# Optimization experiments

Measured on AMD Instinct MI355X. Metric: run time of the kernel, lower is better.

## Reference

```python
import jax, jax.numpy as jnp
import numpy as np

N, E, R = 50000, 400000, 500
X_SIZE = 100
G_SIZE = 100
HID = 64
OUT = 64
HEADS = 2
ALPHA = 0.5
NEG_SLOPE = 0.01  # nn.LeakyReLU default and attention slope
EPS = 1e-12       # F.normalize eps


def _l2norm(x, axis):
    return x / jnp.maximum(jnp.linalg.norm(x, axis=axis, keepdims=True), EPS)


def _xavier(key, shape, gain=1.414):
    fan_in, fan_out = shape[-1], int(np.prod(shape[:-1]))
    std = gain * np.sqrt(2.0 / (fan_in + fan_out))
    return jax.random.normal(key, shape, dtype=jnp.float32) * std


def _att_layer(h, g, row, col, etype, W, b, att, out_size):
    # h: [N, D_h], g: [R, D_g], W: [heads*out, 2*D_h+D_g], att: [1, heads, out]
    n = h.shape[0]
    h_ijk = jnp.concatenate([h[row], h[col], g[etype]], axis=1)      # [E, 2D_h+D_g]
    c_ijk = (h_ijk @ W.T + b).reshape(-1, HEADS, out_size)           # [E, H, O]
    a = jnp.sum(att * c_ijk, axis=2, keepdims=True)                  # [E, H, 1]
    e = jnp.exp(jax.nn.leaky_relu(a, NEG_SLOPE))                     # unnormalized (matches torch exp w/o max-sub)
    denom = jax.ops.segment_sum(e, row, num_segments=n)              # [N, H, 1]
    alpha = e / denom[row]
    # self-edge zeros contribute nothing; segment_sum over num_segments=n is equivalent
    return jax.ops.segment_sum(alpha * c_ijk, col, num_segments=n)   # [N, H, O]


def setup_inputs() -> dict:
    key = jax.random.key(0)
    ks = jax.random.split(key, 20)
    x = jax.random.normal(ks[0], (N, X_SIZE), dtype=jnp.float32)
    g = jax.random.normal(ks[1], (R, G_SIZE), dtype=jnp.float32)
    edge_idx = jax.random.randint(ks[2], (2, E), 0, N)
    edge_type = jax.random.randint(ks[3], (E,), 0, R)
    d1 = 2 * X_SIZE + G_SIZE
    d2 = 2 * HID * HEADS + G_SIZE
    inp = {
        "x": x, "g": g, "edge_idx": edge_idx, "edge_type": edge_type,
        "W1i": _xavier(ks[4], (HEADS * HID, d1)), "b1i": jnp.zeros((HEADS * HID,), jnp.float32),
        "a1i": _xavier(ks[5], (1, HEADS, HID)),
        "W1o": _xavier(ks[6], (HEADS * HID, d1)), "b1o": jnp.zeros((HEADS * HID,), jnp.float32),
        "a1o": _xavier(ks[7], (1, HEADS, HID)),
        "W2i": _xavier(ks[8], (HEADS * OUT, d2)), "b2i": jnp.zeros((HEADS * OUT,), jnp.float32),
        "a2i": _xavier(ks[9], (1, HEADS, OUT)),
        "W2o": _xavier(ks[10], (HEADS * OUT, d2)), "b2o": jnp.zeros((HEADS * OUT,), jnp.float32),
        "a2o": _xavier(ks[11], (1, HEADS, OUT)),
        "We": _xavier(ks[12], (HID, X_SIZE)), "be": jnp.zeros((HID,), jnp.float32),
        "Wr": _xavier(ks[13], (HEADS * HID, G_SIZE)), "br": jnp.zeros((HEADS * HID,), jnp.float32),
    }
    return inp


def reference(x, g, edge_idx, edge_type, W1i, b1i, a1i, W1o, b1o, a1o,
              W2i, b2i, a2i, W2o, b2o, a2o, We, be, Wr, br):
    # x = F.normalize(x, dim=1).detach()
    xn = jax.lax.stop_gradient(_l2norm(x, axis=1))
    row, col = edge_idx[0], edge_idx[1]

    h_in = _att_layer(xn, g, row, col, edge_type, W1i, b1i, a1i, HID)
    h_out = _att_layer(xn, g, col, row, edge_type, W1o, b1o, a1o, HID)
    h = jax.nn.leaky_relu(ALPHA * h_in + (1.0 - ALPHA) * h_out, NEG_SLOPE)
    h = _l2norm(h, axis=2)                                # [N, H, HID]
    h = h.transpose(0, 1, 2).reshape(N, HEADS * HID)      # concat heads

    h_in = _att_layer(h, g, row, col, edge_type, W2i, b2i, a2i, OUT)
    h_out = _att_layer(h, g, col, row, edge_type, W2o, b2o, a2o, OUT)
    h = jax.nn.leaky_relu(ALPHA * h_in + (1.0 - ALPHA) * h_out, NEG_SLOPE)
    h = _l2norm(h, axis=2)                                # [N, H, OUT]

    # EntityLayer: Linear(x)[:, None, :] + h  (requires HID == OUT)
    h_prime = (xn @ We.T + be)[:, None, :] + h            # [N, H, OUT]
    h_prime = h_prime.reshape(N, HEADS * OUT)
    h_prime = _l2norm(h_prime, axis=1)                    # (torch dim=2 bug -> last dim)
    # _merge_heads stores mean but returns input unchanged

    g_prime = g @ Wr.T + br                               # [R, HEADS*HID]
    return h_prime, g_prime
```

## Files before the change

### kernel.cpp

```cpp
#include <hip/hip_runtime.h>

typedef unsigned short u16;
typedef unsigned int u32;
typedef short short8v __attribute__((ext_vector_type(8)));
typedef float float4v __attribute__((ext_vector_type(4)));

#define N_NODES 50000
#define E_EDGES 400000
#define R_REL   500
#define NKEYS   100000
#define SCAN_B  98
#define SEG     ((size_t)N_NODES * 128)

__device__ __forceinline__ float bl(u32 u){ return __uint_as_float(u << 16); }
__device__ __forceinline__ float bh(u32 u){ return __uint_as_float(u & 0xffff0000u); }
__device__ __forceinline__ u16 f2b(float f){
    u32 u = __float_as_uint(f);
    return (u16)((u + 0x7fffu + ((u >> 16) & 1u)) >> 16);
}
__device__ __forceinline__ u32 pk2(float a, float b){ return (u32)f2b(a) | ((u32)f2b(b) << 16); }
__device__ __forceinline__ float lrelu(float x){ return x > 0.f ? x : 0.01f * x; }

__global__ void k_norm_x(const float* __restrict__ x, u16* __restrict__ xnb){
    int wid = threadIdx.x >> 6, l = threadIdx.x & 63;
    int n = blockIdx.x * 4 + wid;
    if (n >= N_NODES) return;
    float v0 = x[(size_t)n * 100 + l];
    float v1 = (l + 64 < 100) ? x[(size_t)n * 100 + 64 + l] : 0.f;
    float ss = v0 * v0 + v1 * v1;
    #pragma unroll
    for (int m = 32; m; m >>= 1) ss += __shfl_xor(ss, m);
    float s = 1.f / fmaxf(sqrtf(ss), 1e-12f);
    xnb[(size_t)n * 128 + l] = f2b(v0 * s);
    xnb[(size_t)n * 128 + 64 + l] = (l + 64 < 100) ? f2b(v1 * s) : (u16)0;
}

__global__ void k_build_wcat(const float* __restrict__ W1i, const float* __restrict__ W1o,
                             const float* __restrict__ W2i, const float* __restrict__ W2o,
                             const float* __restrict__ We,
                             u16* __restrict__ wc1, u16* __restrict__ wc2){
    int idx = blockIdx.x * blockDim.x + threadIdx.x;
    if (idx < 576 * 128){
        int r = idx >> 7, k = idx & 127;
        float v = 0.f;
        if (r < 512){
            int seg = r >> 7, rr = r & 127;
            const float* W = (seg < 2) ? W1i : W1o;
            int off = (seg & 1) ? 100 : 0;
            if (k < 100) v = W[(size_t)rr * 300 + off + k];
        } else {
            int rr = r - 512;
            if (k < 100) v = We[(size_t)rr * 100 + k];
        }
        wc1[idx] = f2b(v);
    } else if (idx < 576 * 128 + 512 * 128){
        int j = idx - 576 * 128;
        int r = j >> 7, k = j & 127;
        int seg = r >> 7, rr = r & 127;
        const float* W = (seg < 2) ? W2i : W2o;
        int off = (seg & 1) ? 128 : 0;
        wc2[j] = f2b(W[(size_t)rr * 356 + off + k]);
    }
}

__global__ void k_pg(const float* __restrict__ g,
                     const float* __restrict__ W1i, const float* __restrict__ W1o,
                     const float* __restrict__ W2i, const float* __restrict__ W2o,
                     const float* __restrict__ b1i, const float* __restrict__ b1o,
                     const float* __restrict__ b2i, const float* __restrict__ b2o,
                     const float* __restrict__ a1i, const float* __restrict__ a1o,
                     const float* __restrict__ a2i, const float* __restrict__ a2o,
                     float* __restrict__ Pg, float* __restrict__ qg){
    int bid = blockIdx.x;
    int r = bid >> 2, t = bid & 3;
    const float *W, *b, *att; int ld, off;
    if (t == 0){ W = W1i; ld = 300; off = 200; b = b1i; att = a1i; }
    else if (t == 1){ W = W1o; ld = 300; off = 200; b = b1o; att = a1o; }
    else if (t == 2){ W = W2i; ld = 356; off = 256; b = b2i; att = a2i; }
    else { W = W2o; ld = 356; off = 256; b = b2o; att = a2o; }
    __shared__ float gs[100];
    __shared__ float red[128];
    int j = threadIdx.x;
    if (j < 100) gs[j] = g[(size_t)r * 100 + j];
    __syncthreads();
    float acc = b[j];
    #pragma unroll 4
    for (int k = 0; k < 100; ++k) acc += gs[k] * W[(size_t)j * ld + off + k];
    Pg[((size_t)t * R_REL + r) * 128 + j] = acc;
    red[j] = att[j] * acc;
    __syncthreads();
    if (j < 2){
        float s = 0.f;
        for (int k = 0; k < 64; ++k) s += red[j * 64 + k];
        qg[((size_t)t * R_REL + r) * 2 + j] = s;
    }
}

__global__ void k_gprime(const float* __restrict__ g, const float* __restrict__ Wr,
                         const float* __restrict__ br, float* __restrict__ out){
    int r = blockIdx.x, j = threadIdx.x;
    __shared__ float gs[100];
    if (j < 100) gs[j] = g[(size_t)r * 100 + j];
    __syncthreads();
    float acc = br[j];
    #pragma unroll 4
    for (int k = 0; k < 100; ++k) acc += gs[k] * Wr[(size_t)j * 100 + k];
    out[(size_t)N_NODES * 128 + (size_t)r * 128 + j] = acc;
}

__launch_bounds__(256)
__global__ void k_gemm(const u16* __restrict__ A, const u16* __restrict__ W,
                       u16* __restrict__ NPt, int M, int NN){
    int l = threadIdx.x & 63, w = threadIdx.x >> 6;
    int rb = blockIdx.x * 64 + w * 16;
    int ar = rb + (l & 15); if (ar >= M) ar = M - 1;
    const u16* Ap = A + (size_t)ar * 128 + (l >> 4) * 8;
    short8v a0 = *(const short8v*)(Ap);
    short8v a1 = *(const short8v*)(Ap + 32);
    short8v a2 = *(const short8v*)(Ap + 64);
    short8v a3 = *(const short8v*)(Ap + 96);
    int ntc = NN >> 4;
    for (int nt = 0; nt < ntc; ++nt){
        const u16* Wp = W + (size_t)(nt * 16 + (l & 15)) * 128 + (l >> 4) * 8;
        short8v b0 = *(const short8v*)(Wp);
        short8v b1 = *(const short8v*)(Wp + 32);
        short8v b2 = *(const short8v*)(Wp + 64);
        short8v b3 = *(const short8v*)(Wp + 96);
        float4v acc = {0.f, 0.f, 0.f, 0.f};
        acc = __builtin_amdgcn_mfma_f32_16x16x32_bf16(a0, b0, acc, 0, 0, 0);
        acc = __builtin_amdgcn_mfma_f32_16x16x32_bf16(a1, b1, acc, 0, 0, 0);
        acc = __builtin_amdgcn_mfma_f32_16x16x32_bf16(a2, b2, acc, 0, 0, 0);
        acc = __builtin_amdgcn_mfma_f32_16x16x32_bf16(a3, b3, acc, 0, 0, 0);
        int cc = nt * 16 + (l & 15);
        int seg = cc >> 7;
        int rr0 = rb + (l >> 4) * 4;
        #pragma unroll
        for (int r = 0; r < 4; ++r){
            int rr = rr0 + r;
            if (rr < M){
                if (seg < 4) NPt[(size_t)seg * SEG + (size_t)rr * 128 + (cc & 127)] = f2b(acc[r]);
                else         NPt[4 * SEG + (size_t)rr * 64 + (cc & 63)] = f2b(acc[r]);
            }
        }
    }
}

__global__ void k_qnode(const u16* __restrict__ NPt,
                        const float* __restrict__ attI, const float* __restrict__ attO,
                        float* __restrict__ q){
    int wid = threadIdx.x >> 6, l = threadIdx.x & 63;
    int n = blockIdx.x * 4 + wid;
    if (n >= N_NODES) return;
    int t = l >> 4, h = (l >> 3) & 1;
    uint4 uv = *(const uint4*)(NPt + (size_t)t * SEG + (size_t)n * 128 + (l & 15) * 8);
    const float* att = ((t < 2) ? attI : attO) + h * 64 + (l & 7) * 8;
    float s = bl(uv.x) * att[0] + bh(uv.x) * att[1] + bl(uv.y) * att[2] + bh(uv.y) * att[3]
            + bl(uv.z) * att[4] + bh(uv.z) * att[5] + bl(uv.w) * att[6] + bh(uv.w) * att[7];
    s += __shfl_xor(s, 1); s += __shfl_xor(s, 2); s += __shfl_xor(s, 4);
    if ((l & 7) == 0) q[(size_t)n * 8 + t * 2 + h] = s;
}

__global__ void k_hist(const int* __restrict__ ei, u32* __restrict__ cnt){
    int e = blockIdx.x * blockDim.x + threadIdx.x;
    if (e >= E_EDGES) return;
    atomicAdd(&cnt[ei[E_EDGES + e]], 1u);
    atomicAdd(&cnt[N_NODES + ei[e]], 1u);
}

__launch_bounds__(1024)
__global__ void k_scan1(const u32* __restrict__ cnt, u32* __restrict__ off, u32* __restrict__ bsum){
    __shared__ u32 sh[1024];
    int t = threadIdx.x, b = blockIdx.x, idx = b * 1024 + t;
    u32 v = cnt[idx];
    sh[t] = v; __syncthreads();
    #pragma unroll
    for (int d = 1; d < 1024; d <<= 1){
        u32 add = (t >= d) ? sh[t - d] : 0;
        __syncthreads();
        sh[t] += add;
        __syncthreads();
    }
    off[idx] = sh[t] - v;
    if (t == 1023) bsum[b] = sh[1023];
}

__global__ void k_scan2(u32* __restrict__ bsum){
    if (threadIdx.x == 0){
        u32 run = 0;
        for (int i = 0; i < SCAN_B; ++i){ u32 t = bsum[i]; bsum[i] = run; run += t; }
    }
}

__launch_bounds__(1024)
__global__ void k_scan3(u32* __restrict__ off, const u32* __restrict__ bsum){
    int idx = blockIdx.x * 1024 + threadIdx.x;
    off[idx] += bsum[blockIdx.x];
}

__global__ void k_pos(const int* __restrict__ ei, const int* __restrict__ ety,
                      u32* __restrict__ cur,
                      u32* __restrict__ Pso, u32* __restrict__ Pss){
    int e = blockIdx.x * blockDim.x + threadIdx.x;
    if (e >= E_EDGES) return;
    u32 row = (u32)ei[e], col = (u32)ei[E_EDGES + e];
    u32 etb = (u32)ety[e] << 20;
    u32 pI = atomicAdd(&cur[col], 1u);
    Pso[pI] = row | etb;  Pss[pI] = col;
    u32 pO = atomicAdd(&cur[N_NODES + row], 1u);
    Pso[pO] = col | etb;  Pss[pO] = row;
}

__global__ void k_edgeA(const u32* __restrict__ Pso, const u32* __restrict__ Pss,
                        const float* __restrict__ q,
                        const float* __restrict__ qgI, const float* __restrict__ qgO,
                        float2* __restrict__ exI, float2* __restrict__ exO){
    int p = blockIdx.x * blockDim.x + threadIdx.x;
    if (p >= 2 * E_EDGES) return;
    u32 so = Pso[p], self = Pss[p];
    u32 oth = so & 0xFFFFF, et = so >> 20;
    u32 row, col;
    if (p < E_EDGES){ row = oth; col = self; } else { row = self; col = oth; }
    const float* qr = q + (size_t)row * 8;
    const float* qc = q + (size_t)col * 8;
    float2 ri, ro;
    ri.x = expf(lrelu(qr[0] + qc[2] + qgI[(size_t)et * 2 + 0]));
    ri.y = expf(lrelu(qr[1] + qc[3] + qgI[(size_t)et * 2 + 1]));
    ro.x = expf(lrelu(qc[4] + qr[6] + qgO[(size_t)et * 2 + 0]));
    ro.y = expf(lrelu(qc[5] + qr[7] + qgO[(size_t)et * 2 + 1]));
    exI[p] = ri;
    exO[p] = ro;
}

__global__ void k_denom(const u32* __restrict__ off,
                        const float2* __restrict__ exI, const float2* __restrict__ exO,
                        float* __restrict__ rdI, float* __restrict__ rdO){
    int n = blockIdx.x * blockDim.x + threadIdx.x;
    if (n >= N_NODES) return;
    float s0 = 0.f, s1 = 0.f;
    for (u32 p = off[N_NODES + n]; p < off[N_NODES + n + 1]; ++p){
        float2 v = exI[p]; s0 += v.x; s1 += v.y;
    }
    rdI[(size_t)n * 2 + 0] = (s0 > 0.f) ? 1.f / s0 : 0.f;
    rdI[(size_t)n * 2 + 1] = (s1 > 0.f) ? 1.f / s1 : 0.f;
    float t0 = 0.f, t1 = 0.f;
    for (u32 p = off[n]; p < off[n + 1]; ++p){
        float2 v = exO[p]; t0 += v.x; t1 += v.y;
    }
    rdO[(size_t)n * 2 + 0] = (t0 > 0.f) ? 1.f / t0 : 0.f;
    rdO[(size_t)n * 2 + 1] = (t1 > 0.f) ? 1.f / t1 : 0.f;
}

__launch_bounds__(256)
__global__ void k_agg(const u32* __restrict__ off,
                      const u32* __restrict__ Pso,
                      const float2* __restrict__ exI, const float2* __restrict__ exO,
                      const u16* __restrict__ NPt,
                      const float* __restrict__ PgI, const float* __restrict__ PgO,
                      const float* __restrict__ rdI, const float* __restrict__ rdO,
                      int final_stage,
                      const u16* __restrict__ NPt1, const float* __restrict__ be,
                      u16* __restrict__ h1b, float* __restrict__ out){
    int wid = threadIdx.x >> 6, l = threadIdx.x & 63;
    int n = blockIdx.x * 4 + wid;
    if (n >= N_NODES) return;
    int h = l >> 5, d0 = l * 2;
    const u16* PaI = NPt;
    const u16* PbI = NPt + SEG;
    const u16* PaO = NPt + 2 * SEG;
    const u16* PbO = NPt + 3 * SEG;
    u32 pbi = *(const u32*)(PbI + (size_t)n * 128 + d0);
    u32 pbo = *(const u32*)(PbO + (size_t)n * 128 + d0);

    float a0 = 0.f, a1 = 0.f, sai = 0.f;
    {
        u32 s0 = off[n], deg = off[n + 1] - s0;
        for (u32 base = 0; base < deg; base += 64){
            u32 k = base + (u32)l;
            u32 so = 0u; float w0 = 0.f, w1 = 0.f;
            if (k < deg){
                u32 idx = s0 + k;
                so = __builtin_nontemporal_load(Pso + idx);
                const float* ep = (const float*)exI + (size_t)idx * 2;
                float e0 = __builtin_nontemporal_load(ep);
                float e1 = __builtin_nontemporal_load(ep + 1);
                u32 oth = so & 0xFFFFFu;
                float2 rd2 = *(const float2*)(rdI + (size_t)oth * 2);
                w0 = e0 * rd2.x; w1 = e1 * rd2.y;
            }
            int cnt = (int)((deg - base < 64u) ? (deg - base) : 64u);
            for (int c = 0; c < cnt; c += 8){
                float wj[8]; u32 pa[8]; float2 gv[8];
                #pragma unroll
                for (int j = 0; j < 8; ++j){
                    u32 s = __shfl(so, c + j);
                    float v0 = __shfl(w0, c + j);
                    float v1 = __shfl(w1, c + j);
                    u32 oth = s & 0xFFFFFu, et = s >> 20;
                    pa[j] = *(const u32*)(PaI + (size_t)oth * 128 + d0);
                    gv[j] = *(const float2*)(PgI + (size_t)et * 128 + d0);
                    wj[j] = h ? v1 : v0;
                }
                #pragma unroll
                for (int j = 0; j < 8; ++j){
                    a0 += wj[j] * (bl(pa[j]) + gv[j].x);
                    a1 += wj[j] * (bh(pa[j]) + gv[j].y);
                    sai += wj[j];
                }
            }
        }
    }
    a0 += sai * bl(pbi);
    a1 += sai * bh(pbi);

    float b0 = 0.f, b1 = 0.f, sao = 0.f;
    {
        u32 s0 = off[N_NODES + n], deg = off[N_NODES + n + 1] - s0;
        for (u32 base = 0; base < deg; base += 64){
            u32 k = base + (u32)l;
            u32 so = 0u; float w0 = 0.f, w1 = 0.f;
            if (k < deg){
                u32 idx = s0 + k;
                so = __builtin_nontemporal_load(Pso + idx);
                const float* ep = (const float*)exO + (size_t)idx * 2;
                float e0 = __builtin_nontemporal_load(ep);
                float e1 = __builtin_nontemporal_load(ep + 1);
                u32 oth = so & 0xFFFFFu;
                float2 rd2 = *(const float2*)(rdO + (size_t)oth * 2);
                w0 = e0 * rd2.x; w1 = e1 * rd2.y;
            }
            int cnt = (int)((deg - base < 64u) ? (deg - base) : 64u);
            for (int c = 0; c < cnt; c += 8){
                float wj[8]; u32 pa[8]; float2 gv[8];
                #pragma unroll
                for (int j = 0; j < 8; ++j){
                    u32 s = __shfl(so, c + j);
                    float v0 = __shfl(w0, c + j);
                    float v1 = __shfl(w1, c + j);
                    u32 oth = s & 0xFFFFFu, et = s >> 20;
                    pa[j] = *(const u32*)(PaO + (size_t)oth * 128 + d0);
                    gv[j] = *(const float2*)(PgO + (size_t)et * 128 + d0);
                    wj[j] = h ? v1 : v0;
                }
                #pragma unroll
                for (int j = 0; j < 8; ++j){
                    b0 += wj[j] * (bl(pa[j]) + gv[j].x);
                    b1 += wj[j] * (bh(pa[j]) + gv[j].y);
                    sao += wj[j];
                }
            }
        }
    }
    b0 += sao * bl(pbo);
    b1 += sao * bh(pbo);

    float vx = lrelu(0.5f * (a0 + b0));
    float vy = lrelu(0.5f * (a1 + b1));
    float ss = vx * vx + vy * vy;
    #pragma unroll
    for (int m = 16; m; m >>= 1) ss += __shfl_xor(ss, m);
    float s2 = 1.f / fmaxf(sqrtf(ss), 1e-12f);
    if (!final_stage){
        *(u32*)(h1b + (size_t)n * 128 + d0) = pk2(vx * s2, vy * s2);
    } else {
        float h20 = vx * s2, h21 = vy * s2;
        int o0 = d0 & 63;
        u32 ue = *(const u32*)(NPt1 + 4 * SEG + (size_t)n * 64 + o0);
        float hp0 = bl(ue) + be[o0] + h20;
        float hp1 = bh(ue) + be[o0 + 1] + h21;
        float st = hp0 * hp0 + hp1 * hp1;
        #pragma unroll
        for (int m = 32; m; m >>= 1) st += __shfl_xor(st, m);
        float s = 1.f / fmaxf(sqrtf(st), 1e-12f);
        float2 o; o.x = hp0 * s; o.y = hp1 * s;
        *(float2*)(out + (size_t)n * 128 + d0) = o;
    }
}

extern "C" void kernel_launch(void* const* d_in, const int* in_sizes, int n_in,
                              void* d_out, int out_size, void* d_ws, size_t ws_size,
                              hipStream_t stream){
    const float* x   = (const float*)d_in[0];
    const float* g   = (const float*)d_in[1];
    const int*   ei  = (const int*)d_in[2];
    const int*   ety = (const int*)d_in[3];
    const float* W1i = (const float*)d_in[4];
    const float* b1i = (const float*)d_in[5];
    const float* a1i = (const float*)d_in[6];
    const float* W1o = (const float*)d_in[7];
    const float* b1o = (const float*)d_in[8];
    const float* a1o = (const float*)d_in[9];
    const float* W2i = (const float*)d_in[10];
    const float* b2i = (const float*)d_in[11];
    const float* a2i = (const float*)d_in[12];
    const float* W2o = (const float*)d_in[13];
    const float* b2o = (const float*)d_in[14];
    const float* a2o = (const float*)d_in[15];
    const float* We  = (const float*)d_in[16];
    const float* be  = (const float*)d_in[17];
    const float* Wr  = (const float*)d_in[18];
    const float* br  = (const float*)d_in[19];
    float* out = (float*)d_out;

    char* ws = (char*)d_ws;
    size_t off_b = 0;
    auto carve = [&](size_t bytes) -> char* {
        char* p = ws + off_b;
        off_b += (bytes + 255) & ~(size_t)255;
        return p;
    };
    u16*    xnb  = (u16*)carve((size_t)N_NODES * 128 * 2);
    u16*    wc1  = (u16*)carve((size_t)576 * 128 * 2);
    u16*    wc2  = (u16*)carve((size_t)512 * 128 * 2);
    u16*    NPt1 = (u16*)carve((SEG * 4 + (size_t)N_NODES * 64) * 2);
    u16*    NPt2 = (u16*)carve(SEG * 4 * 2);
    u16*    h1b  = (u16*)carve((size_t)N_NODES * 128 * 2);
    float*  q    = (float*)carve((size_t)N_NODES * 8 * 4);
    float*  Pg   = (float*)carve((size_t)4 * R_REL * 128 * 4);
    float*  qg   = (float*)carve((size_t)4 * R_REL * 2 * 4);
    u32*    cnt  = (u32*)carve((size_t)SCAN_B * 1024 * 4);
    u32*    offA = (u32*)carve((size_t)SCAN_B * 1024 * 4);
    u32*    cur  = (u32*)carve((size_t)NKEYS * 4);
    u32*    bsum = (u32*)carve((size_t)SCAN_B * 4);
    u32*    Pso  = (u32*)carve((size_t)2 * E_EDGES * 4);
    u32*    Pss  = (u32*)carve((size_t)2 * E_EDGES * 4);
    float2* exI  = (float2*)carve((size_t)2 * E_EDGES * 8);
    float2* exO  = (float2*)carve((size_t)2 * E_EDGES * 8);
    float*  rdI  = (float*)carve((size_t)N_NODES * 2 * 4);
    float*  rdO  = (float*)carve((size_t)N_NODES * 2 * 4);

    hipMemsetAsync(cnt, 0, (size_t)SCAN_B * 1024 * 4, stream);
    k_hist<<<1563, 256, 0, stream>>>(ei, cnt);
    k_scan1<<<SCAN_B, 1024, 0, stream>>>(cnt, offA, bsum);
    k_scan2<<<1, 64, 0, stream>>>(bsum);
    k_scan3<<<SCAN_B, 1024, 0, stream>>>(offA, bsum);
    hipMemcpyAsync(cur, offA, (size_t)NKEYS * 4, hipMemcpyDeviceToDevice, stream);
    k_pos<<<1563, 256, 0, stream>>>(ei, ety, cur, Pso, Pss);

    k_norm_x<<<12500, 256, 0, stream>>>(x, xnb);
    k_build_wcat<<<544, 256, 0, stream>>>(W1i, W1o, W2i, W2o, We, wc1, wc2);
    k_pg<<<2000, 128, 0, stream>>>(g, W1i, W1o, W2i, W2o, b1i, b1o, b2i, b2o,
                                   a1i, a1o, a2i, a2o, Pg, qg);
    k_gprime<<<500, 128, 0, stream>>>(g, Wr, br, out);

    k_gemm<<<782, 256, 0, stream>>>(xnb, wc1, NPt1, N_NODES, 576);
    k_qnode<<<12500, 256, 0, stream>>>(NPt1, a1i, a1o, q);
    k_edgeA<<<3125, 256, 0, stream>>>(Pso, Pss, q, qg, qg + R_REL * 2, exI, exO);
    k_denom<<<196, 256, 0, stream>>>(offA, exI, exO, rdI, rdO);
    k_agg<<<12500, 256, 0, stream>>>(offA, Pso, exI, exO, NPt1, Pg, Pg + R_REL * 128,
                                     rdI, rdO, 0, NPt1, be, h1b, out);

    k_gemm<<<782, 256, 0, stream>>>(h1b, wc2, NPt2, N_NODES, 512);
    k_qnode<<<12500, 256, 0, stream>>>(NPt2, a2i, a2o, q);
    k_edgeA<<<3125, 256, 0, stream>>>(Pso, Pss, q, qg + 2 * R_REL * 2, qg + 3 * R_REL * 2,
                                      exI, exO);
    k_denom<<<196, 256, 0, stream>>>(offA, exI, exO, rdI, rdO);
    k_agg<<<12500, 256, 0, stream>>>(offA, Pso, exI, exO, NPt2, Pg + 2 * R_REL * 128,
                                     Pg + 3 * R_REL * 128, rdI, rdO, 1, NPt1, be, h1b, out);
}
```

Measured before the change: 451.3 us.

## Fuse node attention scores into GEMM and recompute edge exponentials on the fly

Computes the per-node attention dot products (q) inside the MFMA GEMM epilogue using a concatenated attention vector, which removes the separate k_qnode pass. It also drops the k_edgeA kernel and the materialized exI/exO and Pss edge arrays. Edge exponentials are instead recomputed from q and qg inside k_denom and k_agg. This saves two launches and several large edge-sized memory round trips, at the cost of extra random gathers of q and duplicated expf work, plus packing the weights to bf16 before shuffling.

Result: slower. 461.3 us (+2.2%).

```diff
diff --git a/kernel.cpp b/kernel.cpp
--- a/kernel.cpp
+++ b/kernel.cpp
@@ -38,7 +38,10 @@
 __global__ void k_build_wcat(const float* __restrict__ W1i, const float* __restrict__ W1o,
                              const float* __restrict__ W2i, const float* __restrict__ W2o,
                              const float* __restrict__ We,
-                             u16* __restrict__ wc1, u16* __restrict__ wc2){
+                             const float* __restrict__ a1i, const float* __restrict__ a1o,
+                             const float* __restrict__ a2i, const float* __restrict__ a2o,
+                             u16* __restrict__ wc1, u16* __restrict__ wc2,
+                             float* __restrict__ attcat){
     int idx = blockIdx.x * blockDim.x + threadIdx.x;
     if (idx < 576 * 128){
         int r = idx >> 7, k = idx & 127;
@@ -60,6 +63,11 @@
         const float* W = (seg < 2) ? W2i : W2o;
         int off = (seg & 1) ? 128 : 0;
         wc2[j] = f2b(W[(size_t)rr * 356 + off + k]);
+    } else if (idx < 576 * 128 + 512 * 128 + 1024){
+        int j = idx - (576 * 128 + 512 * 128);
+        int s = j >> 9, cc = j & 511;
+        const float* a = s ? ((cc < 256) ? a2i : a2o) : ((cc < 256) ? a1i : a1o);
+        attcat[j] = a[cc & 127];
     }
 }
 
@@ -110,7 +118,8 @@
 
 __launch_bounds__(256)
 __global__ void k_gemm(const u16* __restrict__ A, const u16* __restrict__ W,
-                       u16* __restrict__ NPt, int M, int NN){
+                       const float* __restrict__ attcat,
+                       u16* __restrict__ NPt, float* __restrict__ q, int M, int NN){
     int l = threadIdx.x & 63, w = threadIdx.x >> 6;
     int rb = blockIdx.x * 64 + w * 16;
     int ar = rb + (l & 15); if (ar >= M) ar = M - 1;
@@ -119,6 +128,7 @@
     short8v a1 = *(const short8v*)(Ap + 32);
     short8v a2 = *(const short8v*)(Ap + 64);
     short8v a3 = *(const short8v*)(Ap + 96);
+    float qa[4] = {0.f, 0.f, 0.f, 0.f};
     int ntc = NN >> 4;
     for (int nt = 0; nt < ntc; ++nt){
         const u16* Wp = W + (size_t)(nt * 16 + (l & 15)) * 128 + (l >> 4) * 8;
@@ -142,22 +152,26 @@
                 else         NPt[4 * SEG + (size_t)rr * 64 + (cc & 63)] = f2b(acc[r]);
             }
         }
-    }
-}
-
-__global__ void k_qnode(const u16* __restrict__ NPt,
-                        const float* __restrict__ attI, const float* __restrict__ attO,
-                        float* __restrict__ q){
-    int wid = threadIdx.x >> 6, l = threadIdx.x & 63;
-    int n = blockIdx.x * 4 + wid;
-    if (n >= N_NODES) return;
-    int t = l >> 4, h = (l >> 3) & 1;
-    uint4 uv = *(const uint4*)(NPt + (size_t)t * SEG + (size_t)n * 128 + (l & 15) * 8);
-    const float* att = ((t < 2) ? attI : attO) + h * 64 + (l & 7) * 8;
-    float s = bl(uv.x) * att[0] + bh(uv.x) * att[1] + bl(uv.y) * att[2] + bh(uv.y) * att[3]
-            + bl(uv.z) * att[4] + bh(uv.z) * att[5] + bl(uv.w) * att[6] + bh(uv.w) * att[7];
-    s += __shfl_xor(s, 1); s += __shfl_xor(s, 2); s += __shfl_xor(s, 4);
-    if ((l & 7) == 0) q[(size_t)n * 8 + t * 2 + h] = s;
+        int g = nt >> 2;
+        if (g < 8){
+            float av = attcat[cc];
+            #pragma unroll
+            for (int r = 0; r < 4; ++r) qa[r] += av * acc[r];
+            if ((nt & 3) == 3){
+                #pragma unroll
+                for (int r = 0; r < 4; ++r){
+                    float s = qa[r];
+                    s += __shfl_xor(s, 1); s += __shfl_xor(s, 2);
+                    s += __shfl_xor(s, 4); s += __shfl_xor(s, 8);
+                    if ((l & 15) == 0){
+                        int rr = rr0 + r;
+                        if (rr < M) q[(size_t)rr * 8 + g] = s;
+                    }
+                    qa[r] = 0.f;
+                }
+            }
+        }
+    }
 }
 
 __global__ void k_hist(const int* __restrict__ ei, u32* __restrict__ cnt){
@@ -198,62 +212,51 @@
 }
 
 __global__ void k_pos(const int* __restrict__ ei, const int* __restrict__ ety,
-                      u32* __restrict__ cur,
-                      u32* __restrict__ Pso, u32* __restrict__ Pss){
+                      u32* __restrict__ cur, u32* __restrict__ Pso){
     int e = blockIdx.x * blockDim.x + threadIdx.x;
     if (e >= E_EDGES) return;
     u32 row = (u32)ei[e], col = (u32)ei[E_EDGES + e];
     u32 etb = (u32)ety[e] << 20;
     u32 pI = atomicAdd(&cur[col], 1u);
-    Pso[pI] = row | etb;  Pss[pI] = col;
+    Pso[pI] = row | etb;
     u32 pO = atomicAdd(&cur[N_NODES + row], 1u);
-    Pso[pO] = col | etb;  Pss[pO] = row;
-}
-
-__global__ void k_edgeA(const u32* __restrict__ Pso, const u32* __restrict__ Pss,
+    Pso[pO] = col | etb;
+}
+
+__global__ void k_denom(const u32* __restrict__ off, const u32* __restrict__ Pso,
                         const float* __restrict__ q,
                         const float* __restrict__ qgI, const float* __restrict__ qgO,
-                        float2* __restrict__ exI, float2* __restrict__ exO){
-    int p = blockIdx.x * blockDim.x + threadIdx.x;
-    if (p >= 2 * E_EDGES) return;
-    u32 so = Pso[p], self = Pss[p];
-    u32 oth = so & 0xFFFFF, et = so >> 20;
-    u32 row, col;
-    if (p < E_EDGES){ row = oth; col = self; } else { row = self; col = oth; }
-    const float* qr = q + (size_t)row * 8;
-    const float* qc = q + (size_t)col * 8;
-    float2 ri, ro;
-    ri.x = expf(lrelu(qr[0] + qc[2] + qgI[(size_t)et * 2 + 0]));
-    ri.y = expf(lrelu(qr[1] + qc[3] + qgI[(size_t)et * 2 + 1]));
-    ro.x = expf(lrelu(qc[4] + qr[6] + qgO[(size_t)et * 2 + 0]));
-    ro.y = expf(lrelu(qc[5] + qr[7] + qgO[(size_t)et * 2 + 1]));
-    exI[p] = ri;
-    exO[p] = ro;
-}
-
-__global__ void k_denom(const u32* __restrict__ off,
-                        const float2* __restrict__ exI, const float2* __restrict__ exO,
                         float* __restrict__ rdI, float* __restrict__ rdO){
     int n = blockIdx.x * blockDim.x + threadIdx.x;
     if (n >= N_NODES) return;
+    const float* qn = q + (size_t)n * 8;
+    float qn0 = qn[0], qn1 = qn[1], qn4 = qn[4], qn5 = qn[5];
     float s0 = 0.f, s1 = 0.f;
     for (u32 p = off[N_NODES + n]; p < off[N_NODES + n + 1]; ++p){
-        float2 v = exI[p]; s0 += v.x; s1 += v.y;
+        u32 so = Pso[p]; u32 oth = so & 0xFFFFFu, et = so >> 20;
+        float2 qo = *(const float2*)(q + (size_t)oth * 8 + 2);
+        float2 gq = *(const float2*)(qgI + (size_t)et * 2);
+        s0 += expf(lrelu(qn0 + qo.x + gq.x));
+        s1 += expf(lrelu(qn1 + qo.y + gq.y));
     }
     rdI[(size_t)n * 2 + 0] = (s0 > 0.f) ? 1.f / s0 : 0.f;
     rdI[(size_t)n * 2 + 1] = (s1 > 0.f) ? 1.f / s1 : 0.f;
     float t0 = 0.f, t1 = 0.f;
     for (u32 p = off[n]; p < off[n + 1]; ++p){
-        float2 v = exO[p]; t0 += v.x; t1 += v.y;
+        u32 so = Pso[p]; u32 oth = so & 0xFFFFFu, et = so >> 20;
+        float2 qo = *(const float2*)(q + (size_t)oth * 8 + 6);
+        float2 gq = *(const float2*)(qgO + (size_t)et * 2);
+        t0 += expf(lrelu(qn4 + qo.x + gq.x));
+        t1 += expf(lrelu(qn5 + qo.y + gq.y));
     }
     rdO[(size_t)n * 2 + 0] = (t0 > 0.f) ? 1.f / t0 : 0.f;
     rdO[(size_t)n * 2 + 1] = (t1 > 0.f) ? 1.f / t1 : 0.f;
 }
 
 __launch_bounds__(256)
-__global__ void k_agg(const u32* __restrict__ off,
-                      const u32* __restrict__ Pso,
-                      const float2* __restrict__ exI, const float2* __restrict__ exO,
+__global__ void k_agg(const u32* __restrict__ off, const u32* __restrict__ Pso,
+                      const float* __restrict__ q,
+                      const float* __restrict__ qgI, const float* __restrict__ qgO,
                       const u16* __restrict__ NPt,
                       const float* __restrict__ PgI, const float* __restrict__ PgO,
                       const float* __restrict__ rdI, const float* __restrict__ rdO,
@@ -270,22 +273,25 @@
     const u16* PbO = NPt + 3 * SEG;
     u32 pbi = *(const u32*)(PbI + (size_t)n * 128 + d0);
     u32 pbo = *(const u32*)(PbO + (size_t)n * 128 + d0);
+    float2 qn2 = *(const float2*)(q + (size_t)n * 8 + 2);
+    float2 qn6 = *(const float2*)(q + (size_t)n * 8 + 6);
 
     float a0 = 0.f, a1 = 0.f, sai = 0.f;
     {
         u32 s0 = off[n], deg = off[n + 1] - s0;
         for (u32 base = 0; base < deg; base += 64){
             u32 k = base + (u32)l;
-            u32 so = 0u; float w0 = 0.f, w1 = 0.f;
+            u32 so = 0u, wp = 0u;
             if (k < deg){
                 u32 idx = s0 + k;
                 so = __builtin_nontemporal_load(Pso + idx);
-                const float* ep = (const float*)exI + (size_t)idx * 2;
-                float e0 = __builtin_nontemporal_load(ep);
-                float e1 = __builtin_nontemporal_load(ep + 1);
-                u32 oth = so & 0xFFFFFu;
+                u32 oth = so & 0xFFFFFu, et = so >> 20;
+                float2 qo = *(const float2*)(q + (size_t)oth * 8);
+                float2 gq = *(const float2*)(qgI + (size_t)et * 2);
                 float2 rd2 = *(const float2*)(rdI + (size_t)oth * 2);
-                w0 = e0 * rd2.x; w1 = e1 * rd2.y;
+                float w0 = expf(lrelu(qo.x + qn2.x + gq.x)) * rd2.x;
+                float w1 = expf(lrelu(qo.y + qn2.y + gq.y)) * rd2.y;
+                wp = pk2(w0, w1);
             }
             int cnt = (int)((deg - base < 64u) ? (deg - base) : 64u);
             for (int c = 0; c < cnt; c += 8){
@@ -293,12 +299,11 @@
                 #pragma unroll
                 for (int j = 0; j < 8; ++j){
                     u32 s = __shfl(so, c + j);
-                    float v0 = __shfl(w0, c + j);
-                    float v1 = __shfl(w1, c + j);
+                    u32 wv = __shfl(wp, c + j);
                     u32 oth = s & 0xFFFFFu, et = s >> 20;
                     pa[j] = *(const u32*)(PaI + (size_t)oth * 128 + d0);
                     gv[j] = *(const float2*)(PgI + (size_t)et * 128 + d0);
-                    wj[j] = h ? v1 : v0;
+                    wj[j] = h ? bh(wv) : bl(wv);
                 }
                 #pragma unroll
                 for (int j = 0; j < 8; ++j){
@@ -317,16 +322,17 @@
         u32 s0 = off[N_NODES + n], deg = off[N_NODES + n + 1] - s0;
         for (u32 base = 0; base < deg; base += 64){
             u32 k = base + (u32)l;
-            u32 so = 0u; float w0 = 0.f, w1 = 0.f;
+            u32 so = 0u, wp = 0u;
             if (k < deg){
                 u32 idx = s0 + k;
                 so = __builtin_nontemporal_load(Pso + idx);
-                const float* ep = (const float*)exO + (size_t)idx * 2;
-                float e0 = __builtin_nontemporal_load(ep);
-                float e1 = __builtin_nontemporal_load(ep + 1);
-                u32 oth = so & 0xFFFFFu;
+                u32 oth = so & 0xFFFFFu, et = so >> 20;
+                float2 qo = *(const float2*)(q + (size_t)oth * 8 + 4);
+                float2 gq = *(const float2*)(qgO + (size_t)et * 2);
                 float2 rd2 = *(const float2*)(rdO + (size_t)oth * 2);
-                w0 = e0 * rd2.x; w1 = e1 * rd2.y;
+                float w0 = expf(lrelu(qo.x + qn6.x + gq.x)) * rd2.x;
+                float w1 = expf(lrelu(qo.y + qn6.y + gq.y)) * rd2.y;
+                wp = pk2(w0, w1);
             }
             int cnt = (int)((deg - base < 64u) ? (deg - base) : 64u);
             for (int c = 0; c < cnt; c += 8){
@@ -334,12 +340,11 @@
                 #pragma unroll
                 for (int j = 0; j < 8; ++j){
                     u32 s = __shfl(so, c + j);
-                    float v0 = __shfl(w0, c + j);
-                    float v1 = __shfl(w1, c + j);
+                    u32 wv = __shfl(wp, c + j);
                     u32 oth = s & 0xFFFFFu, et = s >> 20;
                     pa[j] = *(const u32*)(PaO + (size_t)oth * 128 + d0);
                     gv[j] = *(const float2*)(PgO + (size_t)et * 128 + d0);
-                    wj[j] = h ? v1 : v0;
+                    wj[j] = h ? bh(wv) : bl(wv);
                 }
                 #pragma unroll
                 for (int j = 0; j < 8; ++j){
@@ -408,25 +413,23 @@
         off_b += (bytes + 255) & ~(size_t)255;
         return p;
     };
-    u16*    xnb  = (u16*)carve((size_t)N_NODES * 128 * 2);
-    u16*    wc1  = (u16*)carve((size_t)576 * 128 * 2);
-    u16*    wc2  = (u16*)carve((size_t)512 * 128 * 2);
-    u16*    NPt1 = (u16*)carve((SEG * 4 + (size_t)N_NODES * 64) * 2);
-    u16*    NPt2 = (u16*)carve(SEG * 4 * 2);
-    u16*    h1b  = (u16*)carve((size_t)N_NODES * 128 * 2);
-    float*  q    = (float*)carve((size_t)N_NODES * 8 * 4);
-    float*  Pg   = (float*)carve((size_t)4 * R_REL * 128 * 4);
-    float*  qg   = (float*)carve((size_t)4 * R_REL * 2 * 4);
-    u32*    cnt  = (u32*)carve((size_t)SCAN_B * 1024 * 4);
-    u32*    offA = (u32*)carve((size_t)SCAN_B * 1024 * 4);
-    u32*    cur  = (u32*)carve((size_t)NKEYS * 4);
-    u32*    bsum = (u32*)carve((size_t)SCAN_B * 4);
-    u32*    Pso  = (u32*)carve((size_t)2 * E_EDGES * 4);
-    u32*    Pss  = (u32*)carve((size_t)2 * E_EDGES * 4);
-    float2* exI  = (float2*)carve((size_t)2 * E_EDGES * 8);
-    float2* exO  = (float2*)carve((size_t)2 * E_EDGES * 8);
-    float*  rdI  = (float*)carve((size_t)N_NODES * 2 * 4);
-    float*  rdO  = (float*)carve((size_t)N_NODES * 2 * 4);
+    u16*    xnb   = (u16*)carve((size_t)N_NODES * 128 * 2);
+    u16*    wc1   = (u16*)carve((size_t)576 * 128 * 2);
+    u16*    wc2   = (u16*)carve((size_t)512 * 128 * 2);
+    float*  attct = (float*)carve((size_t)1024 * 4);
+    u16*    NPt1  = (u16*)carve((SEG * 4 + (size_t)N_NODES * 64) * 2);
+    u16*    NPt2  = (u16*)carve(SEG * 4 * 2);
+    u16*    h1b   = (u16*)carve((size_t)N_NODES * 128 * 2);
+    float*  q     = (float*)carve((size_t)N_NODES * 8 * 4);
+    float*  Pg    = (float*)carve((size_t)4 * R_REL * 128 * 4);
+    float*  qg    = (float*)carve((size_t)4 * R_REL * 2 * 4);
+    u32*    cnt   = (u32*)carve((size_t)SCAN_B * 1024 * 4);
+    u32*    offA  = (u32*)carve((size_t)SCAN_B * 1024 * 4);
+    u32*    cur   = (u32*)carve((size_t)NKEYS * 4);
+    u32*    bsum  = (u32*)carve((size_t)SCAN_B * 4);
+    u32*    Pso   = (u32*)carve((size_t)2 * E_EDGES * 4);
+    float*  rdI   = (float*)carve((size_t)N_NODES * 2 * 4);
+    float*  rdO   = (float*)carve((size_t)N_NODES * 2 * 4);
 
     hipMemsetAsync(cnt, 0, (size_t)SCAN_B * 1024 * 4, stream);
     k_hist<<<1563, 256, 0, stream>>>(ei, cnt);
@@ -434,26 +437,25 @@
     k_scan2<<<1, 64, 0, stream>>>(bsum);
     k_scan3<<<SCAN_B, 1024, 0, stream>>>(offA, bsum);
     hipMemcpyAsync(cur, offA, (size_t)NKEYS * 4, hipMemcpyDeviceToDevice, stream);
-    k_pos<<<1563, 256, 0, stream>>>(ei, ety, cur, Pso, Pss);
+    k_pos<<<1563, 256, 0, stream>>>(ei, ety, cur, Pso);
 
     k_norm_x<<<12500, 256, 0, stream>>>(x, xnb);
-    k_build_wcat<<<544, 256, 0, stream>>>(W1i, W1o, W2i, W2o, We, wc1, wc2);
+    k_build_wcat<<<548, 256, 0, stream>>>(W1i, W1o, W2i, W2o, We,
+                                          a1i, a1o, a2i, a2o, wc1, wc2, attct);
     k_pg<<<2000, 128, 0, stream>>>(g, W1i, W1o, W2i, W2o, b1i, b1o, b2i, b2o,
                                    a1i, a1o, a2i, a2o, Pg, qg);
     k_gprime<<<500, 128, 0, stream>>>(g, Wr, br, out);
 
-    k_gemm<<<782, 256, 0, stream>>>(xnb, wc1, NPt1, N_NODES, 576);
-    k_qnode<<<12500, 256, 0, stream>>>(NPt1, a1i, a1o, q);
-    k_edgeA<<<3125, 256, 0, stream>>>(Pso, Pss, q, qg, qg + R_REL * 2, exI, exO);
-    k_denom<<<196, 256, 0, stream>>>(offA, exI, exO, rdI, rdO);
-    k_agg<<<12500, 256, 0, stream>>>(offA, Pso, exI, exO, NPt1, Pg, Pg + R_REL * 128,
+    k_gemm<<<782, 256, 0, stream>>>(xnb, wc1, attct, NPt1, q, N_NODES, 576);
+    k_denom<<<196, 256, 0, stream>>>(offA, Pso, q, qg, qg + R_REL * 2, rdI, rdO);
+    k_agg<<<12500, 256, 0, stream>>>(offA, Pso, q, qg, qg + R_REL * 2,
+                                     NPt1, Pg, Pg + R_REL * 128,
                                      rdI, rdO, 0, NPt1, be, h1b, out);
 
-    k_gemm<<<782, 256, 0, stream>>>(h1b, wc2, NPt2, N_NODES, 512);
-    k_qnode<<<12500, 256, 0, stream>>>(NPt2, a2i, a2o, q);
-    k_edgeA<<<3125, 256, 0, stream>>>(Pso, Pss, q, qg + 2 * R_REL * 2, qg + 3 * R_REL * 2,
-                                      exI, exO);
-    k_denom<<<196, 256, 0, stream>>>(offA, exI, exO, rdI, rdO);
-    k_agg<<<12500, 256, 0, stream>>>(offA, Pso, exI, exO, NPt2, Pg + 2 * R_REL * 128,
-                                     Pg + 3 * R_REL * 128, rdI, rdO, 1, NPt1, be, h1b, out);
-}
+    k_gemm<<<782, 256, 0, stream>>>(h1b, wc2, attct + 512, NPt2, q, N_NODES, 512);
+    k_denom<<<196, 256, 0, stream>>>(offA, Pso, q, qg + 2 * R_REL * 2, qg + 3 * R_REL * 2,
+                                     rdI, rdO);
+    k_agg<<<12500, 256, 0, stream>>>(offA, Pso, q, qg + 2 * R_REL * 2, qg + 3 * R_REL * 2,
+                                     NPt2, Pg + 2 * R_REL * 128, Pg + 3 * R_REL * 128,
+                                     rdI, rdO, 1, NPt1, be, h1b, out);
+}
```
